# Optimization experiments

Hardware: AMD Instinct MI355X
Metric: run time of the kernel (lower is better)

Reference implementation:

```python
import jax, jax.numpy as jnp
import numpy as np

QMIN_A, QMAX_A = -128, 127  # int8 activation range
GROUPSIZE = 32


def per_token_quant_dequant(x):
    """Dynamic per-token asymmetric int8 fake-quant (torchao per_token_dynamic_quant)."""
    min_val = jnp.minimum(jnp.min(x, axis=-1, keepdims=True), 0.0)
    max_val = jnp.maximum(jnp.max(x, axis=-1, keepdims=True), 0.0)
    scale = (max_val - min_val) / float(QMAX_A - QMIN_A)
    scale = jnp.maximum(scale, jnp.finfo(x.dtype).eps)
    zp = jnp.clip(QMIN_A - jnp.round(min_val / scale), QMIN_A, QMAX_A)
    q = jnp.clip(jnp.round(x / scale) + zp, QMIN_A, QMAX_A)
    return (q - zp) * scale


def dequant_int4_grouped(w_int, w_scales, w_zeros):
    """w_int: [O, I] int4 values in [-8, 7]; scales/zeros: [O, I//GROUPSIZE]."""
    O, I = w_int.shape
    G = I // GROUPSIZE
    wg = w_int.reshape(O, G, GROUPSIZE).astype(w_scales.dtype)
    w_dq = (wg - w_zeros[:, :, None]) * w_scales[:, :, None]
    return w_dq.reshape(O, I)


def setup_inputs() -> dict:
    key = jax.random.key(0)
    k1, k2, k3 = jax.random.split(key, 3)
    B, S, D_IN, D_OUT = 4, 2048, 2048, 2048
    G = D_IN // GROUPSIZE
    x = jax.random.normal(k1, (B, S, D_IN), dtype=jnp.float32)
    w_int = jax.random.randint(k2, (D_OUT, D_IN), -8, 8, dtype=jnp.int32)
    w_scales = jax.random.uniform(k3, (D_OUT, G), dtype=jnp.float32) * 0.01 + 1e-3
    w_zeros = jnp.zeros((D_OUT, G), dtype=jnp.float32)
    return {"x": x, "w_int": w_int, "w_scales": w_scales, "w_zeros": w_zeros}


def reference(x, w_int, w_scales, w_zeros):
    x_dq = per_token_quant_dequant(x)                  # [B, S, I]
    w_dq = dequant_int4_grouped(w_int, w_scales, w_zeros)  # [O, I]
    return jnp.einsum("bsi,oi->bso", x_dq, w_dq)       # [B, S, O]
```

## Files before the change

kernel.cpp:

```cpp
#include <hip/hip_runtime.h>

#define M_DIM 8192
#define N_DIM 2048
#define K_DIM 2048

#define BM 256
#define BN 256
#define BK 64
#define NT (K_DIM / BK)

#define AS1 __attribute__((address_space(1)))
#define AS3 __attribute__((address_space(3)))

typedef float f32x4 __attribute__((ext_vector_type(4)));
typedef short s16x8 __attribute__((ext_vector_type(8)));

__device__ __forceinline__ unsigned short f2bf(float f) {
  unsigned int u = __float_as_uint(f);
  u += 0x7FFFu + ((u >> 16) & 1u);
  return (unsigned short)(u >> 16);
}

__global__ __launch_bounds__(256) void prep_kernel(
    const float* __restrict__ x, const int* __restrict__ w,
    const float* __restrict__ ws, const float* __restrict__ wz,
    unsigned short* __restrict__ A, unsigned short* __restrict__ W) {
  const int tid = threadIdx.x;
  if (blockIdx.x < M_DIM) {
    const int t = blockIdx.x;
    const float4* r4 = (const float4*)(x + (size_t)t * K_DIM);
    float4 v0 = r4[tid];
    float4 v1 = r4[tid + 256];

    float mn = fminf(fminf(fminf(v0.x, v0.y), fminf(v0.z, v0.w)),
                     fminf(fminf(v1.x, v1.y), fminf(v1.z, v1.w)));
    float mx = fmaxf(fmaxf(fmaxf(v0.x, v0.y), fmaxf(v0.z, v0.w)),
                     fmaxf(fmaxf(v1.x, v1.y), fmaxf(v1.z, v1.w)));
#pragma unroll
    for (int off = 32; off > 0; off >>= 1) {
      mn = fminf(mn, __shfl_xor(mn, off));
      mx = fmaxf(mx, __shfl_xor(mx, off));
    }
    __shared__ float smn[4], smx[4];
    if ((tid & 63) == 0) { smn[tid >> 6] = mn; smx[tid >> 6] = mx; }
    __syncthreads();
    mn = fminf(fminf(smn[0], smn[1]), fminf(smn[2], smn[3]));
    mx = fmaxf(fmaxf(smx[0], smx[1]), fmaxf(smx[2], smx[3]));
    mn = fminf(mn, 0.0f);
    mx = fmaxf(mx, 0.0f);

    float scale = (mx - mn) / 255.0f;
    scale = fmaxf(scale, 1.1920928955078125e-07f);
    const float inv = 1.0f / scale;
    float zp = -128.0f - rintf(mn * inv);
    zp = fminf(fmaxf(zp, -128.0f), 127.0f);

    ushort4* Ao = (ushort4*)(A + (size_t)t * K_DIM);
    {
      float q; ushort4 r;
      q = rintf(v0.x * inv) + zp; q = fminf(fmaxf(q, -128.f), 127.f); r.x = f2bf((q - zp) * scale);
      q = rintf(v0.y * inv) + zp; q = fminf(fmaxf(q, -128.f), 127.f); r.y = f2bf((q - zp) * scale);
      q = rintf(v0.z * inv) + zp; q = fminf(fmaxf(q, -128.f), 127.f); r.z = f2bf((q - zp) * scale);
      q = rintf(v0.w * inv) + zp; q = fminf(fmaxf(q, -128.f), 127.f); r.w = f2bf((q - zp) * scale);
      Ao[tid] = r;
    }
    {
      float q; ushort4 r;
      q = rintf(v1.x * inv) + zp; q = fminf(fmaxf(q, -128.f), 127.f); r.x = f2bf((q - zp) * scale);
      q = rintf(v1.y * inv) + zp; q = fminf(fmaxf(q, -128.f), 127.f); r.y = f2bf((q - zp) * scale);
      q = rintf(v1.z * inv) + zp; q = fminf(fmaxf(q, -128.f), 127.f); r.z = f2bf((q - zp) * scale);
      q = rintf(v1.w * inv) + zp; q = fminf(fmaxf(q, -128.f), 127.f); r.w = f2bf((q - zp) * scale);
      Ao[tid + 256] = r;
    }
  } else {
    const int idx = (blockIdx.x - M_DIM) * 256 + tid;
    const int o  = idx >> 8;
    const int ii = (idx & 255) * 8;
    const int g  = ii >> 5;
    const float s = ws[o * 64 + g];
    const float z = wz[o * 64 + g];
    const int4* wp = (const int4*)(w + (size_t)o * K_DIM + ii);
    int4 a = wp[0], b = wp[1];
    ushort4 r0, r1;
    r0.x = f2bf(((float)a.x - z) * s);
    r0.y = f2bf(((float)a.y - z) * s);
    r0.z = f2bf(((float)a.z - z) * s);
    r0.w = f2bf(((float)a.w - z) * s);
    r1.x = f2bf(((float)b.x - z) * s);
    r1.y = f2bf(((float)b.y - z) * s);
    r1.z = f2bf(((float)b.z - z) * s);
    r1.w = f2bf(((float)b.w - z) * s);
    ushort4* Wo = (ushort4*)(W + (size_t)o * K_DIM + ii);
    Wo[0] = r0;
    Wo[1] = r1;
  }
}


#define PHASE_BAR()                                  \
  do {                                               \
    __builtin_amdgcn_sched_barrier(0);               \
    __builtin_amdgcn_s_barrier();                    \
    __builtin_amdgcn_sched_barrier(0);               \
  } while (0)

#define READ_AF(MH)                                                         \
  do {                                                                      \
    _Pragma("unroll") for (int i = 0; i < 4; ++i) {                         \
      _Pragma("unroll") for (int kk = 0; kk < 2; ++kk) {                    \
        af[i][kk] = *(const s16x8*)&Ab[aoff[(MH) * 4 + i] ^ (kk * 32)];     \
      }                                                                     \
    }                                                                       \
  } while (0)

#define READ_BF(NH)                                                         \
  do {                                                                      \
    _Pragma("unroll") for (int j = 0; j < 2; ++j) {                         \
      _Pragma("unroll") for (int kk = 0; kk < 2; ++kk) {                    \
        bf[NH][j][kk] = *(const s16x8*)&Bb[boff[(NH) * 2 + j] ^ (kk * 32)]; \
      }                                                                     \
    }                                                                       \
  } while (0)

#define MFMA_QUAD(MH, NH)                                                   \
  do {                                                                      \
    __builtin_amdgcn_s_setprio(1);                                          \
    _Pragma("unroll") for (int kk = 0; kk < 2; ++kk) {                      \
      _Pragma("unroll") for (int i = 0; i < 4; ++i) {                       \
        _Pragma("unroll") for (int j = 0; j < 2; ++j) {                     \
          acc[(MH) * 4 + i][(NH) * 2 + j] =                                 \
              __builtin_amdgcn_mfma_f32_16x16x32_bf16(                      \
                  af[i][kk], bf[NH][j][kk],                                 \
                  acc[(MH) * 4 + i][(NH) * 2 + j], 0, 0, 0);                \
        }                                                                   \
      }                                                                     \
    }                                                                       \
    __builtin_amdgcn_s_setprio(0);                                          \
  } while (0)

#define STAGE_A_HALF(KN, DSTP, H)                                            \
  do {                                                                       \
    _Pragma("unroll") for (int j = 0; j < 2; ++j) {                          \
      __builtin_amdgcn_global_load_lds(                                      \
          (const AS1 void*)(ag + (size_t)((H) * 2 + j) * 64 * K_DIM + (KN)), \
          (AS3 void*)(&As[(DSTP) * (BM * BK) + ((H) * 2 + j) * 4096 + tid * 8]), \
          16, 0, 0);                                                         \
    }                                                                        \
  } while (0)

#define STAGE_B_HALF(KN, DSTP, H)                                            \
  do {                                                                       \
    _Pragma("unroll") for (int j = 0; j < 2; ++j) {                          \
      __builtin_amdgcn_global_load_lds(                                      \
          (const AS1 void*)(bg + (size_t)((H) * 2 + j) * 64 * K_DIM + (KN)), \
          (AS3 void*)(&Bs[(DSTP) * (BN * BK) + ((H) * 2 + j) * 4096 + tid * 8]), \
          16, 0, 0);                                                         \
    }                                                                        \
  } while (0)

__global__ __launch_bounds__(512, 2) void gemm_kernel(
    const unsigned short* __restrict__ A,
    const unsigned short* __restrict__ B,
    float* __restrict__ C) {
  __shared__ unsigned short As[2 * BM * BK];
  __shared__ unsigned short Bs[2 * BN * BK];

  const int tid = threadIdx.x;
  const int id  = blockIdx.y * 8 + blockIdx.x;
  const int nid = (id & 7) * 32 + (id >> 3);
  const int bm  = (nid >> 3) * BM;
  const int bn  = (nid & 7) * BN;

  const int lane  = tid & 63;
  const int wv    = tid >> 6;
  const int waveM = (wv >> 2) * 128;
  const int waveN = (wv & 3) * 64;
  const int quad  = lane >> 4;
  const int l16   = lane & 15;

  const int trow = tid >> 3;
  const int phys = (tid & 7) ^ (trow & 7);
  const unsigned short* ag = A + (size_t)(bm + trow) * K_DIM + phys * 8;
  const unsigned short* bg = B + (size_t)(bn + trow) * K_DIM + phys * 8;

  int aoff[8], boff[4];
#pragma unroll
  for (int mi = 0; mi < 8; ++mi)
    aoff[mi] = (waveM + mi * 16 + l16) * BK + ((quad ^ (l16 & 7)) * 8);
#pragma unroll
  for (int ni = 0; ni < 4; ++ni)
    boff[ni] = (waveN + ni * 16 + l16) * BK + ((quad ^ (l16 & 7)) * 8);

  f32x4 acc[8][4] = {};

  STAGE_A_HALF(0, 0, 0);
  STAGE_A_HALF(0, 0, 1);
  STAGE_B_HALF(0, 0, 0);
  STAGE_B_HALF(0, 0, 1);
  STAGE_A_HALF(BK, 1, 0);
  __builtin_amdgcn_sched_barrier(0);
  asm volatile("s_waitcnt vmcnt(2)" ::: "memory");
  __builtin_amdgcn_s_barrier();
  __builtin_amdgcn_sched_barrier(0);

  for (int kt = 0; kt < NT; ++kt) {
    const int p = kt & 1;
    const unsigned short* Ab = &As[p * (BM * BK)];
    const unsigned short* Bb = &Bs[p * (BN * BK)];
    const int k1 = (kt + 1) * BK;
    const int k2 = (kt + 2) * BK;
    const bool pf1 = (kt + 1) < NT;
    const bool pf2 = (kt + 2) < NT;

    s16x8 af[4][2];
    s16x8 bf[2][2][2];

    READ_AF(0);
    READ_BF(0);
    if (pf1) {
      STAGE_A_HALF(k1, p ^ 1, 1);
      STAGE_B_HALF(k1, p ^ 1, 0);
    }
    PHASE_BAR();
    MFMA_QUAD(0, 0);
    PHASE_BAR();

    READ_BF(1);
    if (pf1) STAGE_B_HALF(k1, p ^ 1, 1);
    PHASE_BAR();
    MFMA_QUAD(0, 1);
    PHASE_BAR();

    READ_AF(1);
    PHASE_BAR();
    MFMA_QUAD(1, 1);
    PHASE_BAR();

    if (pf2) STAGE_A_HALF(k2, p, 0);
    MFMA_QUAD(1, 0);
    __builtin_amdgcn_sched_barrier(0);
    if (kt < NT - 2) {
      asm volatile("s_waitcnt vmcnt(2)" ::: "memory");
    } else {
      asm volatile("s_waitcnt vmcnt(0)" ::: "memory");
    }
    PHASE_BAR();
  }

#pragma unroll
  for (int mi = 0; mi < 8; ++mi) {
#pragma unroll
    for (int ni = 0; ni < 4; ++ni) {
      const int o = bn + waveN + ni * 16 + l16;
#pragma unroll
      for (int r = 0; r < 4; ++r) {
        const int row = bm + waveM + mi * 16 + quad * 4 + r;
        C[(size_t)row * N_DIM + o] = acc[mi][ni][r];
      }
    }
  }
}

extern "C" void kernel_launch(void* const* d_in, const int* in_sizes, int n_in,
                              void* d_out, int out_size, void* d_ws, size_t ws_size,
                              hipStream_t stream) {
  const float* x        = (const float*)d_in[0];
  const int*   w_int    = (const int*)d_in[1];
  const float* w_scales = (const float*)d_in[2];
  const float* w_zeros  = (const float*)d_in[3];
  float* out = (float*)d_out;

  unsigned short* Aq = (unsigned short*)d_ws;
  unsigned short* Wq = Aq + (size_t)M_DIM * K_DIM;

  const int prep_blocks = M_DIM + (N_DIM * (K_DIM / 8)) / 256;
  prep_kernel<<<prep_blocks, 256, 0, stream>>>(x, w_int, w_scales, w_zeros, Aq, Wq);
  dim3 grid(N_DIM / BN, M_DIM / BM);
  gemm_kernel<<<grid, 512, 0, stream>>>(Aq, Wq, out);
}
```

Measured before the change: 189.0 us.

## Software-pipeline LDS fragment reads across iterations with double-buffered registers

Restructures the GEMM main loop to unroll by two with ping-pong register fragments, prefetching the next tile's first A/B fragments from LDS during the current tile's last MFMA quad. It cuts barriers per K-step from eight to two and uses compile-time LDS offsets (XOR swizzle folded into per-kk base offsets) to reduce address arithmetic. The cost is higher register pressure from the extra fragment buffers, which at 512 threads with 2 blocks/CU may cause spills, plus tighter correctness reasoning about LDS buffer reuse.

New measurement: 192.4 us. About the same (+1.8%).

```diff
diff --git a/kernel.cpp b/kernel.cpp
--- a/kernel.cpp
+++ b/kernel.cpp
@@ -97,45 +97,40 @@
 }
 
 
-#define PHASE_BAR()                                  \
-  do {                                               \
-    __builtin_amdgcn_sched_barrier(0);               \
-    __builtin_amdgcn_s_barrier();                    \
-    __builtin_amdgcn_sched_barrier(0);               \
-  } while (0)
-
-#define READ_AF(MH)                                                         \
-  do {                                                                      \
-    _Pragma("unroll") for (int i = 0; i < 4; ++i) {                         \
-      _Pragma("unroll") for (int kk = 0; kk < 2; ++kk) {                    \
-        af[i][kk] = *(const s16x8*)&Ab[aoff[(MH) * 4 + i] ^ (kk * 32)];     \
-      }                                                                     \
-    }                                                                       \
-  } while (0)
-
-#define READ_BF(NH)                                                         \
-  do {                                                                      \
-    _Pragma("unroll") for (int j = 0; j < 2; ++j) {                         \
-      _Pragma("unroll") for (int kk = 0; kk < 2; ++kk) {                    \
-        bf[NH][j][kk] = *(const s16x8*)&Bb[boff[(NH) * 2 + j] ^ (kk * 32)]; \
-      }                                                                     \
-    }                                                                       \
-  } while (0)
-
-#define MFMA_QUAD(MH, NH)                                                   \
-  do {                                                                      \
-    __builtin_amdgcn_s_setprio(1);                                          \
-    _Pragma("unroll") for (int kk = 0; kk < 2; ++kk) {                      \
-      _Pragma("unroll") for (int i = 0; i < 4; ++i) {                       \
-        _Pragma("unroll") for (int j = 0; j < 2; ++j) {                     \
-          acc[(MH) * 4 + i][(NH) * 2 + j] =                                 \
-              __builtin_amdgcn_mfma_f32_16x16x32_bf16(                      \
-                  af[i][kk], bf[NH][j][kk],                                 \
-                  acc[(MH) * 4 + i][(NH) * 2 + j], 0, 0, 0);                \
-        }                                                                   \
-      }                                                                     \
-    }                                                                       \
-    __builtin_amdgcn_s_setprio(0);                                          \
+#define SFENCE() __builtin_amdgcn_sched_barrier(0)
+
+#define RD_A(dst, MH, PLIT)                                                  \
+  do {                                                                       \
+    _Pragma("unroll") for (int i = 0; i < 4; ++i) {                          \
+      _Pragma("unroll") for (int kk = 0; kk < 2; ++kk) {                     \
+        dst[i][kk] = *(const s16x8*)((const char*)As + aoffB[kk] +           \
+                      ((PLIT) * 32768 + ((MH) * 4 + i) * 2048));             \
+      }                                                                      \
+    }                                                                        \
+  } while (0)
+
+#define RD_B(dst, NH, PLIT)                                                  \
+  do {                                                                       \
+    _Pragma("unroll") for (int j = 0; j < 2; ++j) {                          \
+      _Pragma("unroll") for (int kk = 0; kk < 2; ++kk) {                     \
+        dst[j][kk] = *(const s16x8*)((const char*)Bs + boffB[kk] +           \
+                      ((PLIT) * 32768 + ((NH) * 2 + j) * 2048));             \
+      }                                                                      \
+    }                                                                        \
+  } while (0)
+
+#define MFMA_Q(afX, bfX, MH, NH)                                             \
+  do {                                                                       \
+    _Pragma("unroll") for (int kk = 0; kk < 2; ++kk) {                       \
+      _Pragma("unroll") for (int i = 0; i < 4; ++i) {                        \
+        _Pragma("unroll") for (int j = 0; j < 2; ++j) {                      \
+          acc[(MH) * 4 + i][(NH) * 2 + j] =                                  \
+              __builtin_amdgcn_mfma_f32_16x16x32_bf16(                       \
+                  afX[i][kk], bfX[j][kk],                                    \
+                  acc[(MH) * 4 + i][(NH) * 2 + j], 0, 0, 0);                 \
+        }                                                                    \
+      }                                                                      \
+    }                                                                        \
   } while (0)
 
 #define STAGE_A_HALF(KN, DSTP, H)                                            \
@@ -157,6 +152,49 @@
           16, 0, 0);                                                         \
     }                                                                        \
   } while (0)
+
+#define ITER(KT, PLIT, BN0, BN1)                                             \
+  {                                                                          \
+    const int k1 = ((KT) + 1) * BK;                                          \
+    const int k2 = ((KT) + 2) * BK;                                          \
+                                                         \
+    RD_B(BN1, 1, PLIT);                                                      \
+    RD_A(af1, 1, PLIT);                                                      \
+    if ((KT) + 1 < NT) {                                                     \
+      STAGE_A_HALF(k1, (PLIT) ^ 1, 1);                                       \
+      STAGE_B_HALF(k1, (PLIT) ^ 1, 0);                                       \
+      STAGE_B_HALF(k1, (PLIT) ^ 1, 1);                                       \
+    }                                                                        \
+    SFENCE();              \
+    __builtin_amdgcn_s_setprio(1);                                           \
+    MFMA_Q(af0, BN0, 0, 0);                                                  \
+    MFMA_Q(af0, BN1, 0, 1);                                                  \
+    MFMA_Q(af1, BN1, 1, 1);                                                  \
+    __builtin_amdgcn_s_setprio(0);                                           \
+    SFENCE();                                                                \
+    __builtin_amdgcn_s_barrier();             \
+    SFENCE();                                                                \
+                                                         \
+    if ((KT) + 2 < NT) STAGE_A_HALF(k2, PLIT, 0);                            \
+    SFENCE();                                                                \
+    if ((KT) + 2 < NT) {                                                     \
+      asm volatile("s_waitcnt vmcnt(2)" ::: "memory");                       \
+    } else {                                                                 \
+      asm volatile("s_waitcnt vmcnt(0)" ::: "memory");                       \
+    }                                                                        \
+    SFENCE();                                                                \
+    __builtin_amdgcn_s_barrier();            \
+    SFENCE();                                                                \
+                                                         \
+    if ((KT) + 1 < NT) {                                                     \
+      RD_A(af0, 0, (PLIT) ^ 1);                                              \
+      RD_B(BN1, 0, (PLIT) ^ 1);          \
+    }                                                                        \
+    SFENCE();       \
+    __builtin_amdgcn_s_setprio(1);                                           \
+    MFMA_Q(af1, BN0, 1, 0);                                                  \
+    __builtin_amdgcn_s_setprio(0);                                           \
+  }
 
 __global__ __launch_bounds__(512, 2) void gemm_kernel(
     const unsigned short* __restrict__ A,
@@ -183,68 +221,33 @@
   const unsigned short* ag = A + (size_t)(bm + trow) * K_DIM + phys * 8;
   const unsigned short* bg = B + (size_t)(bn + trow) * K_DIM + phys * 8;
 
-  int aoff[8], boff[4];
-#pragma unroll
-  for (int mi = 0; mi < 8; ++mi)
-    aoff[mi] = (waveM + mi * 16 + l16) * BK + ((quad ^ (l16 & 7)) * 8);
-#pragma unroll
-  for (int ni = 0; ni < 4; ++ni)
-    boff[ni] = (waveN + ni * 16 + l16) * BK + ((quad ^ (l16 & 7)) * 8);
+  int aoffB[2], boffB[2];
+#pragma unroll
+  for (int kk = 0; kk < 2; ++kk) {
+    aoffB[kk] = ((waveM + l16) * BK + ((quad ^ (l16 & 7) ^ (kk * 4)) * 8)) * 2;
+    boffB[kk] = ((waveN + l16) * BK + ((quad ^ (l16 & 7) ^ (kk * 4)) * 8)) * 2;
+  }
 
   f32x4 acc[8][4] = {};
+  s16x8 af0[4][2], af1[4][2];
+  s16x8 bX[2][2], bY[2][2];
 
   STAGE_A_HALF(0, 0, 0);
   STAGE_A_HALF(0, 0, 1);
   STAGE_B_HALF(0, 0, 0);
   STAGE_B_HALF(0, 0, 1);
   STAGE_A_HALF(BK, 1, 0);
-  __builtin_amdgcn_sched_barrier(0);
+  SFENCE();
   asm volatile("s_waitcnt vmcnt(2)" ::: "memory");
+  SFENCE();
   __builtin_amdgcn_s_barrier();
-  __builtin_amdgcn_sched_barrier(0);
-
-  for (int kt = 0; kt < NT; ++kt) {
-    const int p = kt & 1;
-    const unsigned short* Ab = &As[p * (BM * BK)];
-    const unsigned short* Bb = &Bs[p * (BN * BK)];
-    const int k1 = (kt + 1) * BK;
-    const int k2 = (kt + 2) * BK;
-    const bool pf1 = (kt + 1) < NT;
-    const bool pf2 = (kt + 2) < NT;
-
-    s16x8 af[4][2];
-    s16x8 bf[2][2][2];
-
-    READ_AF(0);
-    READ_BF(0);
-    if (pf1) {
-      STAGE_A_HALF(k1, p ^ 1, 1);
-      STAGE_B_HALF(k1, p ^ 1, 0);
-    }
-    PHASE_BAR();
-    MFMA_QUAD(0, 0);
-    PHASE_BAR();
-
-    READ_BF(1);
-    if (pf1) STAGE_B_HALF(k1, p ^ 1, 1);
-    PHASE_BAR();
-    MFMA_QUAD(0, 1);
-    PHASE_BAR();
-
-    READ_AF(1);
-    PHASE_BAR();
-    MFMA_QUAD(1, 1);
-    PHASE_BAR();
-
-    if (pf2) STAGE_A_HALF(k2, p, 0);
-    MFMA_QUAD(1, 0);
-    __builtin_amdgcn_sched_barrier(0);
-    if (kt < NT - 2) {
-      asm volatile("s_waitcnt vmcnt(2)" ::: "memory");
-    } else {
-      asm volatile("s_waitcnt vmcnt(0)" ::: "memory");
-    }
-    PHASE_BAR();
+  SFENCE();
+  RD_A(af0, 0, 0);
+  RD_B(bX, 0, 0);
+
+  for (int kt = 0; kt < NT; kt += 2) {
+    ITER(kt, 0, bX, bY);
+    ITER(kt + 1, 1, bY, bX);
   }
 
 #pragma unroll
```
